# Optimization experiments

Measured on AMD Instinct MI355X. Metric: run time of the kernel, lower is better.

Reference implementation:

```python
import jax, jax.numpy as jnp
import numpy as np

N_NODES = 50000
N_GRAPHS = 512
EPS = 1e-5


def _ln(x, g, b):
    mu = jnp.mean(x, axis=-1, keepdims=True)
    var = jnp.var(x, axis=-1, keepdims=True)
    return (x - mu) * jax.lax.rsqrt(var + EPS) * g + b


def _sage(x, src, dst, wl, wr, bl):
    # mean-aggregate neighbor features: messages x[src] -> dst
    s = jax.ops.segment_sum(x[src], dst, num_segments=N_NODES)
    cnt = jax.ops.segment_sum(jnp.ones((src.shape[0],), x.dtype), dst, num_segments=N_NODES)
    agg = s / jnp.maximum(cnt, 1.0)[:, None]
    # PyG SAGEConv: lin_l(agg) + lin_r(x), bias only on lin_l
    return agg @ wl + bl + x @ wr


def setup_inputs() -> dict:
    key = jax.random.key(0)
    ks = jax.random.split(key, 16)
    C, H, NC, E = 128, 128, 2, 800000
    inp = {
        'x': jax.random.normal(ks[0], (N_NODES, C), jnp.float32),
        'edge_index': jax.random.randint(ks[1], (2, E), 0, N_NODES, jnp.int32),
        'batch': jnp.sort(jax.random.randint(ks[2], (N_NODES,), 0, N_GRAPHS, jnp.int32)),
    }
    def w(k, shape):
        return jax.random.normal(k, shape, jnp.float32) * 0.05
    inp.update({
        'w1l': w(ks[3], (C, H)), 'w1r': w(ks[4], (C, H)), 'b1': jnp.zeros((H,), jnp.float32),
        'g1': jnp.ones((H,), jnp.float32), 'be1': jnp.zeros((H,), jnp.float32),
        'w2l': w(ks[5], (H, H)), 'w2r': w(ks[6], (H, H)), 'b2': jnp.zeros((H,), jnp.float32),
        'g2': jnp.ones((H,), jnp.float32), 'be2': jnp.zeros((H,), jnp.float32),
        'w3l': w(ks[7], (H, H)), 'w3r': w(ks[8], (H, H)), 'b3': jnp.zeros((H,), jnp.float32),
        'g3': jnp.ones((H,), jnp.float32), 'be3': jnp.zeros((H,), jnp.float32),
        'wc': w(ks[9], (H, NC)), 'bc': jnp.zeros((NC,), jnp.float32),
    })
    return inp


def reference(x, edge_index, batch, w1l, w1r, b1, g1, be1, w2l, w2r, b2, g2, be2,
              w3l, w3r, b3, g3, be3, wc, bc):
    src, dst = edge_index[0], edge_index[1]
    # eval mode: dropout is identity
    h1 = _ln(jax.nn.relu(_sage(x, src, dst, w1l, w1r, b1)), g1, be1)
    h2 = _ln(jax.nn.relu(_sage(h1, src, dst, w2l, w2r, b2)) + h1, g2, be2)
    h3 = _ln(h2 + jax.nn.relu(_sage(h2, src, dst, w3l, w3r, b3)), g3, be3)
    # global mean pool over graphs
    s = jax.ops.segment_sum(h3, batch, num_segments=N_GRAPHS)
    cnt = jax.ops.segment_sum(jnp.ones((h3.shape[0],), h3.dtype), batch, num_segments=N_GRAPHS)
    avg = s / jnp.maximum(cnt, 1.0)[:, None]
    out = avg @ wc + bc
    return (out, h3, avg)
```

## Files before the change

### kernel.cpp

```cpp
#include <hip/hip_runtime.h>

#define NND 50000
#define NE  800000
#define CF  128
#define NGR 512
#define DCAP 64

typedef __bf16 bf16;
typedef __bf16 bf16x2 __attribute__((ext_vector_type(2)));
typedef __bf16 bf16x4 __attribute__((ext_vector_type(4)));
typedef __bf16 bf16x8 __attribute__((ext_vector_type(8)));
typedef float  f32x4  __attribute__((ext_vector_type(4)));

__device__ __forceinline__ int swz(int n, int k) {
  return n * 256 + (((k >> 3) ^ (n & 31)) << 3) + (k & 7);
}

__global__ __launch_bounds__(256) void conv_k(const float* __restrict__ x,
                                              bf16* __restrict__ xb,
                                              const float* __restrict__ w1l, const float* __restrict__ w1r,
                                              const float* __restrict__ w2l, const float* __restrict__ w2r,
                                              const float* __restrict__ w3l, const float* __restrict__ w3r,
                                              bf16* __restrict__ wb,
                                              const int* __restrict__ batch,
                                              int* __restrict__ gs,
                                              int* __restrict__ cnt) {
  int t = blockIdx.x * 256 + threadIdx.x;
  if (t < (NND * CF / 4)) {
    f32x4 v = ((const f32x4*)x)[t];
    bf16x4 o;
    o[0] = (bf16)v[0]; o[1] = (bf16)v[1]; o[2] = (bf16)v[2]; o[3] = (bf16)v[3];
    ((bf16x4*)xb)[t] = o;
  }
  if (t < 49152) {
    int m = t >> 13, w = t & 8191;
    const float* src = (m == 0) ? w1l : (m == 1) ? w1r : (m == 2) ? w2l
                     : (m == 3) ? w2r : (m == 4) ? w3l : w3r;
    float2 v = *(const float2*)(src + w * 2);
    bf16x2 o;
    o[0] = (bf16)v.x; o[1] = (bf16)v.y;
    ((bf16x2*)wb)[t] = o;
  }
  if (t < NND) {
    cnt[t] = 0;
    int b = batch[t];
    if (t == 0) {
      for (int g = 0; g <= b; g++) gs[g] = 0;
    } else {
      int pb = batch[t - 1];
      for (int g = pb + 1; g <= b; g++) gs[g] = t;
    }
    if (t == NND - 1) {
      for (int g = b + 1; g <= NGR; g++) gs[g] = NND;
    }
  }
}

__global__ __launch_bounds__(256) void fill_k(const int* __restrict__ src,
                                              const int* __restrict__ dst,
                                              int* __restrict__ cnt,
                                              unsigned short* __restrict__ csr) {
  int r  = blockIdx.x & 7;
  int lo = r * 6250, hi = lo + 6250;
  int base = (blockIdx.x >> 3) * 2048 + threadIdx.x * 8;
#pragma unroll
  for (int h = 0; h < 2; h++) {
    int e = base + h * 4;
    if (e < NE) {
      int4 d4 = *(const int4*)(dst + e);
      int dd[4] = {d4.x, d4.y, d4.z, d4.w};
#pragma unroll
      for (int u = 0; u < 4; u++) {
        int d = dd[u];
        if (d >= lo && d < hi) {
          int p = atomicAdd(&cnt[d], 1);
          if (p < DCAP) csr[d * DCAP + p] = (unsigned short)src[e + u];
        }
      }
    }
  }
}

__global__ __launch_bounds__(256) void agg_k(const bf16* __restrict__ xin,
                                             const int* __restrict__ cnt,
                                             const unsigned short* __restrict__ csr,
                                             bf16* __restrict__ aggout) {
  int wid  = (blockIdx.x * 256 + threadIdx.x) >> 6;
  int lane = threadIdx.x & 63;
  if (wid >= NND) return;
  int sub = lane >> 4;
  int c8  = (lane & 15) * 8;
  int deg = min(cnt[wid], DCAP);
  int ebase = wid * DCAP;
  float a[8] = {};
  {
    int s[8]; float m[8]; bf16x8 v[8];
#pragma unroll
    for (int u = 0; u < 4; u++) {
      int i = u * 4 + sub;
      s[u] = csr[ebase + ((i < deg) ? i : 0)];
      m[u] = (i < deg) ? 1.f : 0.f;
    }
#pragma unroll
    for (int u = 0; u < 4; u++) v[u] = *(const bf16x8*)(xin + s[u] * 128 + c8);
    if (deg > 16) {
#pragma unroll
      for (int u = 4; u < 8; u++) {
        int i = u * 4 + sub;
        s[u] = csr[ebase + ((i < deg) ? i : 0)];
        m[u] = (i < deg) ? 1.f : 0.f;
      }
#pragma unroll
      for (int u = 4; u < 8; u++) v[u] = *(const bf16x8*)(xin + s[u] * 128 + c8);
    }
#pragma unroll
    for (int u = 0; u < 4; u++)
#pragma unroll
      for (int j = 0; j < 8; j++) a[j] += m[u] * (float)v[u][j];
    if (deg > 16) {
#pragma unroll
      for (int u = 4; u < 8; u++)
#pragma unroll
        for (int j = 0; j < 8; j++) a[j] += m[u] * (float)v[u][j];
    }
  }
  for (int e = 32; e < deg; e += 16) {
    int s[4]; float m[4]; bf16x8 v[4];
#pragma unroll
    for (int u = 0; u < 4; u++) {
      int i = e + u * 4 + sub;
      s[u] = csr[ebase + ((i < deg) ? i : 0)];
      m[u] = (i < deg) ? 1.f : 0.f;
    }
#pragma unroll
    for (int u = 0; u < 4; u++) v[u] = *(const bf16x8*)(xin + s[u] * 128 + c8);
#pragma unroll
    for (int u = 0; u < 4; u++)
#pragma unroll
      for (int j = 0; j < 8; j++) a[j] += m[u] * (float)v[u][j];
  }
#pragma unroll
  for (int j = 0; j < 8; j++) {
    a[j] += __shfl_xor(a[j], 16);
    a[j] += __shfl_xor(a[j], 32);
  }
  if (sub == 0) {
    float inv = 1.0f / fmaxf((float)deg, 1.0f);
    bf16x8 o;
#pragma unroll
    for (int j = 0; j < 8; j++) o[j] = (bf16)(a[j] * inv);
    *(bf16x8*)(aggout + wid * 128 + c8) = o;
  }
}

template <typename TO>
__global__ __launch_bounds__(256, 2) void gemm_k(
    const bf16* __restrict__ aggp, const bf16* __restrict__ prev,
    const bf16* __restrict__ wl, const bf16* __restrict__ wr,
    const float* __restrict__ bias, const float* __restrict__ gamma,
    const float* __restrict__ beta, TO* __restrict__ outp, int addres) {
  __shared__ bf16 bt[128 * 256];
  int tid = threadIdx.x;
  for (int e = tid; e < 128 * 64; e += 256) {
    int k  = e >> 6;
    int n2 = (e & 63) << 1;
    {
      bf16x2 v = *(const bf16x2*)(wl + k * 128 + n2);
      bt[swz(n2, k)]     = v[0];
      bt[swz(n2 + 1, k)] = v[1];
    }
    {
      bf16x2 v = *(const bf16x2*)(wr + k * 128 + n2);
      bt[swz(n2, k + 128)]     = v[0];
      bt[swz(n2 + 1, k + 128)] = v[1];
    }
  }
  __syncthreads();

  int wave = tid >> 6, lane = tid & 63;
  int q = lane >> 4, r = lane & 15;
  int wrow = blockIdx.x * 128 + wave * 32;

  int arow[2];
#pragma unroll
  for (int rt = 0; rt < 2; rt++) {
    int ar = wrow + rt * 16 + r;
    arow[rt] = (ar < NND) ? ar : (NND - 1);
  }

  f32x4 acc[2][8] = {};

#pragma unroll
  for (int kk = 0; kk < 8; kk++) {
    int kof = kk * 32 + q * 8;
    bf16x8 af[2];
#pragma unroll
    for (int rt = 0; rt < 2; rt++) {
      const bf16* ap = (kk < 4) ? (aggp + arow[rt] * 128 + kof)
                                : (prev + arow[rt] * 128 + (kof - 128));
      af[rt] = *(const bf16x8*)ap;
    }
#pragma unroll
    for (int t = 0; t < 8; t++) {
      int n = t * 16 + r;
      bf16x8 bfrag = *(const bf16x8*)&bt[n * 256 + (((kof >> 3) ^ (n & 31)) << 3)];
#pragma unroll
      for (int rt = 0; rt < 2; rt++)
        acc[rt][t] = __builtin_amdgcn_mfma_f32_16x16x32_bf16(af[rt], bfrag, acc[rt][t], 0, 0, 0);
    }
  }

  float biasf[8], gf[8], bef[8];
#pragma unroll
  for (int t = 0; t < 8; t++) {
    int c = t * 16 + r;
    biasf[t] = bias[c];
    gf[t]    = gamma[c];
    bef[t]   = beta[c];
  }

#pragma unroll
  for (int rt = 0; rt < 2; rt++) {
#pragma unroll
    for (int reg = 0; reg < 4; reg++) {
      int row = wrow + rt * 16 + q * 4 + reg;
      int rr  = (row < NND) ? row : (NND - 1);
      const bf16* prow = prev + rr * 128;
      float vals[8];
      float s = 0.f, s2 = 0.f;
#pragma unroll
      for (int t = 0; t < 8; t++) {
        float v = acc[rt][t][reg] + biasf[t];
        v = fmaxf(v, 0.f);
        if (addres) v += (float)prow[t * 16 + r];
        vals[t] = v;
        s += v;
        s2 += v * v;
      }
#pragma unroll
      for (int m = 1; m < 16; m <<= 1) {
        s  += __shfl_xor(s, m);
        s2 += __shfl_xor(s2, m);
      }
      float mean = s * (1.f / 128.f);
      float var  = fmaxf(s2 * (1.f / 128.f) - mean * mean, 0.f);
      float rstd = rsqrtf(var + 1e-5f);
      if (row < NND) {
        TO* orow = outp + row * 128;
#pragma unroll
        for (int t = 0; t < 8; t++)
          orow[t * 16 + r] = (TO)((vals[t] - mean) * rstd * gf[t] + bef[t]);
      }
    }
  }
}

__global__ __launch_bounds__(256) void poolhead_k(
    const float* __restrict__ h3, const int* __restrict__ gs,
    const float* __restrict__ wc, const float* __restrict__ bc,
    float* __restrict__ outv, float* __restrict__ avgv) {
  int g = blockIdx.x;
  int s = gs[g], epos = gs[g + 1];
  int tid = threadIdx.x;
  int wave = tid >> 6, lane = tid & 63;
  float a0 = 0.f, a1 = 0.f;
  for (int row = s + wave; row < epos; row += 4) {
    float2 v = *(const float2*)(h3 + row * 128 + 2 * lane);
    a0 += v.x; a1 += v.y;
  }
  __shared__ float red[4][128];
  red[wave][2 * lane]     = a0;
  red[wave][2 * lane + 1] = a1;
  __syncthreads();
  __shared__ float sp[4];
  if (tid < 128) {
    float t4  = red[0][tid] + red[1][tid] + red[2][tid] + red[3][tid];
    float inv = 1.f / fmaxf((float)(epos - s), 1.f);
    float avg = t4 * inv;
    avgv[g * 128 + tid] = avg;
    float p0 = avg * wc[tid * 2 + 0];
    float p1 = avg * wc[tid * 2 + 1];
#pragma unroll
    for (int m = 1; m < 64; m <<= 1) {
      p0 += __shfl_xor(p0, m);
      p1 += __shfl_xor(p1, m);
    }
    if ((tid & 63) == 0) {
      sp[(tid >> 6) * 2]     = p0;
      sp[(tid >> 6) * 2 + 1] = p1;
    }
  }
  __syncthreads();
  if (tid == 0) {
    outv[g * 2 + 0] = sp[0] + sp[2] + bc[0];
    outv[g * 2 + 1] = sp[1] + sp[3] + bc[1];
  }
}

extern "C" void kernel_launch(void* const* d_in, const int* in_sizes, int n_in,
                              void* d_out, int out_size, void* d_ws, size_t ws_size,
                              hipStream_t stream) {
  const float* x   = (const float*)d_in[0];
  const int* ei    = (const int*)d_in[1];
  const int* batch = (const int*)d_in[2];
  const float* w1l = (const float*)d_in[3],  *w1r = (const float*)d_in[4];
  const float* b1  = (const float*)d_in[5],  *g1  = (const float*)d_in[6],  *be1 = (const float*)d_in[7];
  const float* w2l = (const float*)d_in[8],  *w2r = (const float*)d_in[9];
  const float* b2  = (const float*)d_in[10], *g2  = (const float*)d_in[11], *be2 = (const float*)d_in[12];
  const float* w3l = (const float*)d_in[13], *w3r = (const float*)d_in[14];
  const float* b3  = (const float*)d_in[15], *g3  = (const float*)d_in[16], *be3 = (const float*)d_in[17];
  const float* wc  = (const float*)d_in[18], *bc  = (const float*)d_in[19];
  const int* srcv = ei;
  const int* dstv = ei + NE;

  char* base = (char*)d_ws;
  int*            cnt  = (int*)(base + 0);
  int*            gs   = (int*)(base + 200064);
  bf16*           wb   = (bf16*)(base + 202752);
  unsigned short* csr  = (unsigned short*)(base + 399360);
  bf16*           agg  = (bf16*)(base + 6799360);
  bf16*           h1   = (bf16*)(base + 19599360);
  bf16*           h2xb = (bf16*)(base + 32399360);

  bf16* wb1l = wb,          *wb1r = wb + 16384;
  bf16* wb2l = wb + 32768,  *wb2r = wb + 49152;
  bf16* wb3l = wb + 65536,  *wb3r = wb + 81920;

  float* outv = (float*)d_out;
  float* h3   = outv + 1024;
  float* avgv = outv + 1024 + NND * CF;

  conv_k<<<6250, 256, 0, stream>>>(x, h2xb, w1l, w1r, w2l, w2r, w3l, w3r, wb, batch, gs, cnt);
  fill_k<<<3128, 256, 0, stream>>>(srcv, dstv, cnt, csr);

  agg_k<<<12500, 256, 0, stream>>>(h2xb, cnt, csr, agg);
  gemm_k<bf16><<<391, 256, 0, stream>>>(agg, h2xb, wb1l, wb1r, b1, g1, be1, h1, 0);
  agg_k<<<12500, 256, 0, stream>>>(h1, cnt, csr, agg);
  gemm_k<bf16><<<391, 256, 0, stream>>>(agg, h1, wb2l, wb2r, b2, g2, be2, h2xb, 1);
  agg_k<<<12500, 256, 0, stream>>>(h2xb, cnt, csr, agg);
  gemm_k<float><<<391, 256, 0, stream>>>(agg, h2xb, wb3l, wb3r, b3, g3, be3, h3, 1);
  poolhead_k<<<NGR, 256, 0, stream>>>(h3, gs, wc, bc, outv, avgv);
}
```

Measured before the change: 312.8 us.

## Fuse graph mean-pool into final GEMM epilogue and merge conversion with CSR fill

The last GEMM kernel now accumulates pooled per-graph sums in shared memory with atomics and flushes them to a global buffer, so pooling no longer needs to re-read h3. A small finish kernel then divides by node counts and applies the classifier head. The conversion and CSR-fill kernels are merged into one launch, with a separate zeroing kernel for the counters and pool buffer, and src is now read with vector loads. This trades an extra pass over h3 and a launch for shared and global float atomics, which add contention and make the summation order nondeterministic.

```diff
diff --git a/kernel.cpp b/kernel.cpp
--- a/kernel.cpp
+++ b/kernel.cpp
@@ -16,65 +16,71 @@
   return n * 256 + (((k >> 3) ^ (n & 31)) << 3) + (k & 7);
 }
 
-__global__ __launch_bounds__(256) void conv_k(const float* __restrict__ x,
-                                              bf16* __restrict__ xb,
-                                              const float* __restrict__ w1l, const float* __restrict__ w1r,
-                                              const float* __restrict__ w2l, const float* __restrict__ w2r,
-                                              const float* __restrict__ w3l, const float* __restrict__ w3r,
-                                              bf16* __restrict__ wb,
-                                              const int* __restrict__ batch,
-                                              int* __restrict__ gs,
-                                              int* __restrict__ cnt) {
-  int t = blockIdx.x * 256 + threadIdx.x;
-  if (t < (NND * CF / 4)) {
-    f32x4 v = ((const f32x4*)x)[t];
-    bf16x4 o;
-    o[0] = (bf16)v[0]; o[1] = (bf16)v[1]; o[2] = (bf16)v[2]; o[3] = (bf16)v[3];
-    ((bf16x4*)xb)[t] = o;
-  }
-  if (t < 49152) {
-    int m = t >> 13, w = t & 8191;
-    const float* src = (m == 0) ? w1l : (m == 1) ? w1r : (m == 2) ? w2l
-                     : (m == 3) ? w2r : (m == 4) ? w3l : w3r;
-    float2 v = *(const float2*)(src + w * 2);
-    bf16x2 o;
-    o[0] = (bf16)v.x; o[1] = (bf16)v.y;
-    ((bf16x2*)wb)[t] = o;
-  }
-  if (t < NND) {
-    cnt[t] = 0;
-    int b = batch[t];
-    if (t == 0) {
-      for (int g = 0; g <= b; g++) gs[g] = 0;
-    } else {
-      int pb = batch[t - 1];
-      for (int g = pb + 1; g <= b; g++) gs[g] = t;
-    }
-    if (t == NND - 1) {
-      for (int g = b + 1; g <= NGR; g++) gs[g] = NND;
-    }
-  }
-}
-
-__global__ __launch_bounds__(256) void fill_k(const int* __restrict__ src,
-                                              const int* __restrict__ dst,
-                                              int* __restrict__ cnt,
-                                              unsigned short* __restrict__ csr) {
-  int r  = blockIdx.x & 7;
-  int lo = r * 6250, hi = lo + 6250;
-  int base = (blockIdx.x >> 3) * 2048 + threadIdx.x * 8;
-#pragma unroll
-  for (int h = 0; h < 2; h++) {
-    int e = base + h * 4;
-    if (e < NE) {
-      int4 d4 = *(const int4*)(dst + e);
-      int dd[4] = {d4.x, d4.y, d4.z, d4.w};
-#pragma unroll
-      for (int u = 0; u < 4; u++) {
-        int d = dd[u];
-        if (d >= lo && d < hi) {
-          int p = atomicAdd(&cnt[d], 1);
-          if (p < DCAP) csr[d * DCAP + p] = (unsigned short)src[e + u];
+__global__ __launch_bounds__(256) void zero_k(int4* __restrict__ p) {
+  p[blockIdx.x * 256 + threadIdx.x] = int4{0, 0, 0, 0};
+}
+
+__global__ __launch_bounds__(256) void convfill_k(const float* __restrict__ x,
+                                                  bf16* __restrict__ xb,
+                                                  const float* __restrict__ w1l, const float* __restrict__ w1r,
+                                                  const float* __restrict__ w2l, const float* __restrict__ w2r,
+                                                  const float* __restrict__ w3l, const float* __restrict__ w3r,
+                                                  bf16* __restrict__ wb,
+                                                  const int* __restrict__ batch,
+                                                  int* __restrict__ gs,
+                                                  const int* __restrict__ src,
+                                                  const int* __restrict__ dst,
+                                                  int* __restrict__ cnt,
+                                                  unsigned short* __restrict__ csr) {
+  if (blockIdx.x < 6250) {
+    int t = blockIdx.x * 256 + threadIdx.x;
+    {
+      f32x4 v = ((const f32x4*)x)[t];
+      bf16x4 o;
+      o[0] = (bf16)v[0]; o[1] = (bf16)v[1]; o[2] = (bf16)v[2]; o[3] = (bf16)v[3];
+      ((bf16x4*)xb)[t] = o;
+    }
+    if (t < 49152) {
+      int m = t >> 13, w = t & 8191;
+      const float* sp = (m == 0) ? w1l : (m == 1) ? w1r : (m == 2) ? w2l
+                      : (m == 3) ? w2r : (m == 4) ? w3l : w3r;
+      float2 v = *(const float2*)(sp + w * 2);
+      bf16x2 o;
+      o[0] = (bf16)v.x; o[1] = (bf16)v.y;
+      ((bf16x2*)wb)[t] = o;
+    }
+    if (t < NND) {
+      int b = batch[t];
+      if (t == 0) {
+        for (int g = 0; g <= b; g++) gs[g] = 0;
+      } else {
+        int pb = batch[t - 1];
+        for (int g = pb + 1; g <= b; g++) gs[g] = t;
+      }
+      if (t == NND - 1) {
+        for (int g = b + 1; g <= NGR; g++) gs[g] = NND;
+      }
+    }
+  } else {
+    int bb = blockIdx.x - 6250;
+    int r  = bb & 7;
+    int lo = r * 6250, hi = lo + 6250;
+    int ebase = (bb >> 3) * 2048;
+#pragma unroll
+    for (int h = 0; h < 2; h++) {
+      int e = ebase + h * 1024 + threadIdx.x * 4;
+      if (e < NE) {
+        int4 d4 = *(const int4*)(dst + e);
+        int4 s4 = *(const int4*)(src + e);
+        int dd[4] = {d4.x, d4.y, d4.z, d4.w};
+        int ss[4] = {s4.x, s4.y, s4.z, s4.w};
+#pragma unroll
+        for (int u = 0; u < 4; u++) {
+          int d = dd[u];
+          if (d >= lo && d < hi) {
+            int p = atomicAdd(&cnt[d], 1);
+            if (p < DCAP) csr[d * DCAP + p] = (unsigned short)ss[u];
+          }
         }
       }
     }
@@ -158,7 +164,8 @@
     const bf16* __restrict__ aggp, const bf16* __restrict__ prev,
     const bf16* __restrict__ wl, const bf16* __restrict__ wr,
     const float* __restrict__ bias, const float* __restrict__ gamma,
-    const float* __restrict__ beta, TO* __restrict__ outp, int addres) {
+    const float* __restrict__ beta, TO* __restrict__ outp, int addres,
+    const int* __restrict__ batchp, float* __restrict__ avgsum, int dopool) {
   __shared__ bf16 bt[128 * 256];
   int tid = threadIdx.x;
   for (int e = tid; e < 128 * 64; e += 256) {
@@ -210,6 +217,18 @@
     }
   }
 
+  float* poolbuf = (float*)bt;
+  int gmin = 0, gspan = 0;
+  if (dopool) {
+    __syncthreads();
+    int row0 = blockIdx.x * 128;
+    gmin  = batchp[row0];
+    int gmax = batchp[min(row0 + 127, NND - 1)];
+    gspan = gmax - gmin + 1;
+    for (int i = tid; i < gspan * 128; i += 256) poolbuf[i] = 0.f;
+    __syncthreads();
+  }
+
   float biasf[8], gf[8], bef[8];
 #pragma unroll
   for (int t = 0; t < 8; t++) {
@@ -247,48 +266,45 @@
       float rstd = rsqrtf(var + 1e-5f);
       if (row < NND) {
         TO* orow = outp + row * 128;
-#pragma unroll
-        for (int t = 0; t < 8; t++)
-          orow[t * 16 + r] = (TO)((vals[t] - mean) * rstd * gf[t] + bef[t]);
-      }
-    }
-  }
-}
-
-__global__ __launch_bounds__(256) void poolhead_k(
-    const float* __restrict__ h3, const int* __restrict__ gs,
+        int gb = dopool ? batchp[row] : 0;
+#pragma unroll
+        for (int t = 0; t < 8; t++) {
+          float o = (vals[t] - mean) * rstd * gf[t] + bef[t];
+          orow[t * 16 + r] = (TO)o;
+          if (dopool) atomicAdd(&poolbuf[(gb - gmin) * 128 + t * 16 + r], o);
+        }
+      }
+    }
+  }
+
+  if (dopool) {
+    __syncthreads();
+    for (int i = tid; i < gspan * 128; i += 256)
+      atomicAdd(&avgsum[gmin * 128 + i], poolbuf[i]);
+  }
+}
+
+__global__ __launch_bounds__(128) void poolfin_k(
+    const float* __restrict__ avgsum, const int* __restrict__ gs,
     const float* __restrict__ wc, const float* __restrict__ bc,
     float* __restrict__ outv, float* __restrict__ avgv) {
   int g = blockIdx.x;
-  int s = gs[g], epos = gs[g + 1];
   int tid = threadIdx.x;
-  int wave = tid >> 6, lane = tid & 63;
-  float a0 = 0.f, a1 = 0.f;
-  for (int row = s + wave; row < epos; row += 4) {
-    float2 v = *(const float2*)(h3 + row * 128 + 2 * lane);
-    a0 += v.x; a1 += v.y;
-  }
-  __shared__ float red[4][128];
-  red[wave][2 * lane]     = a0;
-  red[wave][2 * lane + 1] = a1;
-  __syncthreads();
+  float s = avgsum[g * 128 + tid];
+  int c = gs[g + 1] - gs[g];
+  float avg = s / fmaxf((float)c, 1.f);
+  avgv[g * 128 + tid] = avg;
+  float p0 = avg * wc[tid * 2 + 0];
+  float p1 = avg * wc[tid * 2 + 1];
+#pragma unroll
+  for (int m = 1; m < 64; m <<= 1) {
+    p0 += __shfl_xor(p0, m);
+    p1 += __shfl_xor(p1, m);
+  }
   __shared__ float sp[4];
-  if (tid < 128) {
-    float t4  = red[0][tid] + red[1][tid] + red[2][tid] + red[3][tid];
-    float inv = 1.f / fmaxf((float)(epos - s), 1.f);
-    float avg = t4 * inv;
-    avgv[g * 128 + tid] = avg;
-    float p0 = avg * wc[tid * 2 + 0];
-    float p1 = avg * wc[tid * 2 + 1];
-#pragma unroll
-    for (int m = 1; m < 64; m <<= 1) {
-      p0 += __shfl_xor(p0, m);
-      p1 += __shfl_xor(p1, m);
-    }
-    if ((tid & 63) == 0) {
-      sp[(tid >> 6) * 2]     = p0;
-      sp[(tid >> 6) * 2 + 1] = p1;
-    }
+  if ((tid & 63) == 0) {
+    sp[(tid >> 6) * 2]     = p0;
+    sp[(tid >> 6) * 2 + 1] = p1;
   }
   __syncthreads();
   if (tid == 0) {
@@ -314,13 +330,14 @@
   const int* dstv = ei + NE;
 
   char* base = (char*)d_ws;
-  int*            cnt  = (int*)(base + 0);
-  int*            gs   = (int*)(base + 200064);
-  bf16*           wb   = (bf16*)(base + 202752);
-  unsigned short* csr  = (unsigned short*)(base + 399360);
-  bf16*           agg  = (bf16*)(base + 6799360);
-  bf16*           h1   = (bf16*)(base + 19599360);
-  bf16*           h2xb = (bf16*)(base + 32399360);
+  int*            cnt    = (int*)(base + 0);
+  float*          avgsum = (float*)(base + 200704);
+  int*            gs     = (int*)(base + 462848);
+  bf16*           wb     = (bf16*)(base + 465408);
+  unsigned short* csr    = (unsigned short*)(base + 662016);
+  bf16*           agg    = (bf16*)(base + 7062016);
+  bf16*           h1     = (bf16*)(base + 19862016);
+  bf16*           h2xb   = (bf16*)(base + 32662016);
 
   bf16* wb1l = wb,          *wb1r = wb + 16384;
   bf16* wb2l = wb + 32768,  *wb2r = wb + 49152;
@@ -330,14 +347,18 @@
   float* h3   = outv + 1024;
   float* avgv = outv + 1024 + NND * CF;
 
-  conv_k<<<6250, 256, 0, stream>>>(x, h2xb, w1l, w1r, w2l, w2r, w3l, w3r, wb, batch, gs, cnt);
-  fill_k<<<3128, 256, 0, stream>>>(srcv, dstv, cnt, csr);
+  zero_k<<<113, 256, 0, stream>>>((int4*)base);
+  convfill_k<<<9378, 256, 0, stream>>>(x, h2xb, w1l, w1r, w2l, w2r, w3l, w3r, wb,
+                                       batch, gs, srcv, dstv, cnt, csr);
 
   agg_k<<<12500, 256, 0, stream>>>(h2xb, cnt, csr, agg);
-  gemm_k<bf16><<<391, 256, 0, stream>>>(agg, h2xb, wb1l, wb1r, b1, g1, be1, h1, 0);
+  gemm_k<bf16><<<391, 256, 0, stream>>>(agg, h2xb, wb1l, wb1r, b1, g1, be1, h1, 0,
+                                        nullptr, nullptr, 0);
   agg_k<<<12500, 256, 0, stream>>>(h1, cnt, csr, agg);
-  gemm_k<bf16><<<391, 256, 0, stream>>>(agg, h1, wb2l, wb2r, b2, g2, be2, h2xb, 1);
+  gemm_k<bf16><<<391, 256, 0, stream>>>(agg, h1, wb2l, wb2r, b2, g2, be2, h2xb, 1,
+                                        nullptr, nullptr, 0);
   agg_k<<<12500, 256, 0, stream>>>(h2xb, cnt, csr, agg);
-  gemm_k<float><<<391, 256, 0, stream>>>(agg, h2xb, wb3l, wb3r, b3, g3, be3, h3, 1);
-  poolhead_k<<<NGR, 256, 0, stream>>>(h3, gs, wc, bc, outv, avgv);
-}
+  gemm_k<float><<<391, 256, 0, stream>>>(agg, h2xb, wb3l, wb3r, b3, g3, be3, h3, 1,
+                                         batch, avgsum, 1);
+  poolfin_k<<<NGR, 128, 0, stream>>>(avgsum, gs, wc, bc, outv, avgv);
+}
```

Result: slower. 339.7 us (+8.6%).

## Pre-swizzle weights once, halve GEMM LDS tile, merge conversion and CSR fill

Applied to the files above, without the earlier changes.

Weights are now written once in the swizzled [n][k] layout during conversion, so each GEMM block only does vectorized copies into LDS. The tile drops to 64 rows with a 32KB LDS buffer, loaded in two halves (lin_l, then lin_r), which allows more resident blocks and twice as many blocks. The conversion and edge-fill kernels are merged into one launch, with a separate zeroing kernel for counts, and the fill now reads src with vectorized loads. The cost is extra syncs between the GEMM halves. The merge also relies on cnt being zeroed by the earlier launch, since the fill blocks in the same grid can no longer depend on it.

```diff
diff --git a/kernel.cpp b/kernel.cpp
--- a/kernel.cpp
+++ b/kernel.cpp
@@ -12,69 +12,73 @@
 typedef __bf16 bf16x8 __attribute__((ext_vector_type(8)));
 typedef float  f32x4  __attribute__((ext_vector_type(4)));
 
-__device__ __forceinline__ int swz(int n, int k) {
-  return n * 256 + (((k >> 3) ^ (n & 31)) << 3) + (k & 7);
-}
-
-__global__ __launch_bounds__(256) void conv_k(const float* __restrict__ x,
-                                              bf16* __restrict__ xb,
-                                              const float* __restrict__ w1l, const float* __restrict__ w1r,
-                                              const float* __restrict__ w2l, const float* __restrict__ w2r,
-                                              const float* __restrict__ w3l, const float* __restrict__ w3r,
-                                              bf16* __restrict__ wb,
-                                              const int* __restrict__ batch,
-                                              int* __restrict__ gs,
-                                              int* __restrict__ cnt) {
-  int t = blockIdx.x * 256 + threadIdx.x;
-  if (t < (NND * CF / 4)) {
-    f32x4 v = ((const f32x4*)x)[t];
-    bf16x4 o;
-    o[0] = (bf16)v[0]; o[1] = (bf16)v[1]; o[2] = (bf16)v[2]; o[3] = (bf16)v[3];
-    ((bf16x4*)xb)[t] = o;
-  }
-  if (t < 49152) {
-    int m = t >> 13, w = t & 8191;
-    const float* src = (m == 0) ? w1l : (m == 1) ? w1r : (m == 2) ? w2l
-                     : (m == 3) ? w2r : (m == 4) ? w3l : w3r;
-    float2 v = *(const float2*)(src + w * 2);
-    bf16x2 o;
-    o[0] = (bf16)v.x; o[1] = (bf16)v.y;
-    ((bf16x2*)wb)[t] = o;
-  }
-  if (t < NND) {
-    cnt[t] = 0;
-    int b = batch[t];
-    if (t == 0) {
-      for (int g = 0; g <= b; g++) gs[g] = 0;
-    } else {
-      int pb = batch[t - 1];
-      for (int g = pb + 1; g <= b; g++) gs[g] = t;
-    }
-    if (t == NND - 1) {
-      for (int g = b + 1; g <= NGR; g++) gs[g] = NND;
-    }
-  }
-}
-
-__global__ __launch_bounds__(256) void fill_k(const int* __restrict__ src,
-                                              const int* __restrict__ dst,
-                                              int* __restrict__ cnt,
-                                              unsigned short* __restrict__ csr) {
-  int r  = blockIdx.x & 7;
-  int lo = r * 6250, hi = lo + 6250;
-  int base = (blockIdx.x >> 3) * 2048 + threadIdx.x * 8;
-#pragma unroll
-  for (int h = 0; h < 2; h++) {
-    int e = base + h * 4;
-    if (e < NE) {
-      int4 d4 = *(const int4*)(dst + e);
-      int dd[4] = {d4.x, d4.y, d4.z, d4.w};
-#pragma unroll
-      for (int u = 0; u < 4; u++) {
-        int d = dd[u];
-        if (d >= lo && d < hi) {
-          int p = atomicAdd(&cnt[d], 1);
-          if (p < DCAP) csr[d * DCAP + p] = (unsigned short)src[e + u];
+__global__ __launch_bounds__(256) void zero_k(int4* __restrict__ p) {
+  p[blockIdx.x * 256 + threadIdx.x] = int4{0, 0, 0, 0};
+}
+
+__global__ __launch_bounds__(256) void convfill_k(const float* __restrict__ x,
+                                                  bf16* __restrict__ xb,
+                                                  const float* __restrict__ w1l, const float* __restrict__ w1r,
+                                                  const float* __restrict__ w2l, const float* __restrict__ w2r,
+                                                  const float* __restrict__ w3l, const float* __restrict__ w3r,
+                                                  bf16* __restrict__ wb,
+                                                  const int* __restrict__ batch,
+                                                  int* __restrict__ gs,
+                                                  const int* __restrict__ src,
+                                                  const int* __restrict__ dst,
+                                                  int* __restrict__ cnt,
+                                                  unsigned short* __restrict__ csr) {
+  if (blockIdx.x < 6250) {
+    int t = blockIdx.x * 256 + threadIdx.x;
+    {
+      f32x4 v = ((const f32x4*)x)[t];
+      bf16x4 o;
+      o[0] = (bf16)v[0]; o[1] = (bf16)v[1]; o[2] = (bf16)v[2]; o[3] = (bf16)v[3];
+      ((bf16x4*)xb)[t] = o;
+    }
+    if (t < 49152) {
+      int m = t >> 13, w2 = t & 8191;
+      const float* sp = (m == 0) ? w1l : (m == 1) ? w1r : (m == 2) ? w2l
+                      : (m == 3) ? w2r : (m == 4) ? w3l : w3r;
+      int e0 = w2 * 2;
+      int k = e0 >> 7, n = e0 & 127;
+      float2 v = *(const float2*)(sp + e0);
+      bf16* wm = wb + m * 16384;
+      wm[n * 128       + ((((k >> 3) ^ (n       & 15)) << 3)) + (k & 7)] = (bf16)v.x;
+      wm[(n + 1) * 128 + ((((k >> 3) ^ ((n + 1) & 15)) << 3)) + (k & 7)] = (bf16)v.y;
+    }
+    if (t < NND) {
+      int b = batch[t];
+      if (t == 0) {
+        for (int g = 0; g <= b; g++) gs[g] = 0;
+      } else {
+        int pb = batch[t - 1];
+        for (int g = pb + 1; g <= b; g++) gs[g] = t;
+      }
+      if (t == NND - 1) {
+        for (int g = b + 1; g <= NGR; g++) gs[g] = NND;
+      }
+    }
+  } else {
+    int bb = blockIdx.x - 6250;
+    int r  = bb & 7;
+    int lo = r * 6250, hi = lo + 6250;
+    int ebase = (bb >> 3) * 2048;
+#pragma unroll
+    for (int h = 0; h < 2; h++) {
+      int e = ebase + h * 1024 + threadIdx.x * 4;
+      if (e < NE) {
+        int4 d4 = *(const int4*)(dst + e);
+        int4 s4 = *(const int4*)(src + e);
+        int dd[4] = {d4.x, d4.y, d4.z, d4.w};
+        int ss[4] = {s4.x, s4.y, s4.z, s4.w};
+#pragma unroll
+        for (int u = 0; u < 4; u++) {
+          int d = dd[u];
+          if (d >= lo && d < hi) {
+            int p = atomicAdd(&cnt[d], 1);
+            if (p < DCAP) csr[d * DCAP + p] = (unsigned short)ss[u];
+          }
         }
       }
     }
@@ -154,59 +158,61 @@
 }
 
 template <typename TO>
-__global__ __launch_bounds__(256, 2) void gemm_k(
+__global__ __launch_bounds__(256, 4) void gemm_k(
     const bf16* __restrict__ aggp, const bf16* __restrict__ prev,
-    const bf16* __restrict__ wl, const bf16* __restrict__ wr,
+    const bf16* __restrict__ wswz,
     const float* __restrict__ bias, const float* __restrict__ gamma,
     const float* __restrict__ beta, TO* __restrict__ outp, int addres) {
-  __shared__ bf16 bt[128 * 256];
+  __shared__ bf16 bt[16384];
   int tid = threadIdx.x;
-  for (int e = tid; e < 128 * 64; e += 256) {
-    int k  = e >> 6;
-    int n2 = (e & 63) << 1;
-    {
-      bf16x2 v = *(const bf16x2*)(wl + k * 128 + n2);
-      bt[swz(n2, k)]     = v[0];
-      bt[swz(n2 + 1, k)] = v[1];
-    }
-    {
-      bf16x2 v = *(const bf16x2*)(wr + k * 128 + n2);
-      bt[swz(n2, k + 128)]     = v[0];
-      bt[swz(n2 + 1, k + 128)] = v[1];
-    }
-  }
-  __syncthreads();
-
-  int wave = tid >> 6, lane = tid & 63;
+  int lane = tid & 63;
+  int wave = tid >> 6;
   int q = lane >> 4, r = lane & 15;
-  int wrow = blockIdx.x * 128 + wave * 32;
-
-  int arow[2];
-#pragma unroll
-  for (int rt = 0; rt < 2; rt++) {
-    int ar = wrow + rt * 16 + r;
-    arow[rt] = (ar < NND) ? ar : (NND - 1);
-  }
-
-  f32x4 acc[2][8] = {};
-
-#pragma unroll
-  for (int kk = 0; kk < 8; kk++) {
-    int kof = kk * 32 + q * 8;
-    bf16x8 af[2];
-#pragma unroll
-    for (int rt = 0; rt < 2; rt++) {
-      const bf16* ap = (kk < 4) ? (aggp + arow[rt] * 128 + kof)
-                                : (prev + arow[rt] * 128 + (kof - 128));
-      af[rt] = *(const bf16x8*)ap;
-    }
+  int wrow = blockIdx.x * 64 + wave * 16;
+  int arow = min(wrow + r, NND - 1);
+
+  {
+    const bf16x8* g = (const bf16x8*)wswz;
+#pragma unroll
+    for (int i = 0; i < 8; i++)
+      ((bf16x8*)bt)[tid + i * 256] = g[tid + i * 256];
+  }
+  bf16x8 af0[4], af1[4];
+  {
+    const bf16* a0 = aggp + arow * 128 + q * 8;
+    const bf16* a1 = prev + arow * 128 + q * 8;
+#pragma unroll
+    for (int kk = 0; kk < 4; kk++) af0[kk] = *(const bf16x8*)(a0 + kk * 32);
+#pragma unroll
+    for (int kk = 0; kk < 4; kk++) af1[kk] = *(const bf16x8*)(a1 + kk * 32);
+  }
+  __syncthreads();
+
+  f32x4 acc[8] = {};
+#pragma unroll
+  for (int kk = 0; kk < 4; kk++) {
 #pragma unroll
     for (int t = 0; t < 8; t++) {
       int n = t * 16 + r;
-      bf16x8 bfrag = *(const bf16x8*)&bt[n * 256 + (((kof >> 3) ^ (n & 31)) << 3)];
-#pragma unroll
-      for (int rt = 0; rt < 2; rt++)
-        acc[rt][t] = __builtin_amdgcn_mfma_f32_16x16x32_bf16(af[rt], bfrag, acc[rt][t], 0, 0, 0);
+      bf16x8 bfrag = *(const bf16x8*)&bt[n * 128 + (((kk * 4 + q) ^ (n & 15)) << 3)];
+      acc[t] = __builtin_amdgcn_mfma_f32_16x16x32_bf16(af0[kk], bfrag, acc[t], 0, 0, 0);
+    }
+  }
+  __syncthreads();
+  {
+    const bf16x8* g = (const bf16x8*)(wswz + 16384);
+#pragma unroll
+    for (int i = 0; i < 8; i++)
+      ((bf16x8*)bt)[tid + i * 256] = g[tid + i * 256];
+  }
+  __syncthreads();
+#pragma unroll
+  for (int kk = 0; kk < 4; kk++) {
+#pragma unroll
+    for (int t = 0; t < 8; t++) {
+      int n = t * 16 + r;
+      bf16x8 bfrag = *(const bf16x8*)&bt[n * 128 + (((kk * 4 + q) ^ (n & 15)) << 3)];
+      acc[t] = __builtin_amdgcn_mfma_f32_16x16x32_bf16(af1[kk], bfrag, acc[t], 0, 0, 0);
     }
   }
 
@@ -220,37 +226,34 @@
   }
 
 #pragma unroll
-  for (int rt = 0; rt < 2; rt++) {
-#pragma unroll
-    for (int reg = 0; reg < 4; reg++) {
-      int row = wrow + rt * 16 + q * 4 + reg;
-      int rr  = (row < NND) ? row : (NND - 1);
-      const bf16* prow = prev + rr * 128;
-      float vals[8];
-      float s = 0.f, s2 = 0.f;
-#pragma unroll
-      for (int t = 0; t < 8; t++) {
-        float v = acc[rt][t][reg] + biasf[t];
-        v = fmaxf(v, 0.f);
-        if (addres) v += (float)prow[t * 16 + r];
-        vals[t] = v;
-        s += v;
-        s2 += v * v;
-      }
-#pragma unroll
-      for (int m = 1; m < 16; m <<= 1) {
-        s  += __shfl_xor(s, m);
-        s2 += __shfl_xor(s2, m);
-      }
-      float mean = s * (1.f / 128.f);
-      float var  = fmaxf(s2 * (1.f / 128.f) - mean * mean, 0.f);
-      float rstd = rsqrtf(var + 1e-5f);
-      if (row < NND) {
-        TO* orow = outp + row * 128;
-#pragma unroll
-        for (int t = 0; t < 8; t++)
-          orow[t * 16 + r] = (TO)((vals[t] - mean) * rstd * gf[t] + bef[t]);
-      }
+  for (int reg = 0; reg < 4; reg++) {
+    int row = wrow + q * 4 + reg;
+    int rr  = (row < NND) ? row : (NND - 1);
+    const bf16* prow = prev + rr * 128;
+    float vals[8];
+    float s = 0.f, s2 = 0.f;
+#pragma unroll
+    for (int t = 0; t < 8; t++) {
+      float v = acc[t][reg] + biasf[t];
+      v = fmaxf(v, 0.f);
+      if (addres) v += (float)prow[t * 16 + r];
+      vals[t] = v;
+      s += v;
+      s2 += v * v;
+    }
+#pragma unroll
+    for (int m = 1; m < 16; m <<= 1) {
+      s  += __shfl_xor(s, m);
+      s2 += __shfl_xor(s2, m);
+    }
+    float mean = s * (1.f / 128.f);
+    float var  = fmaxf(s2 * (1.f / 128.f) - mean * mean, 0.f);
+    float rstd = rsqrtf(var + 1e-5f);
+    if (row < NND) {
+      TO* orow = outp + row * 128;
+#pragma unroll
+      for (int t = 0; t < 8; t++)
+        orow[t * 16 + r] = (TO)((vals[t] - mean) * rstd * gf[t] + bef[t]);
     }
   }
 }
@@ -315,29 +318,26 @@
 
   char* base = (char*)d_ws;
   int*            cnt  = (int*)(base + 0);
-  int*            gs   = (int*)(base + 200064);
-  bf16*           wb   = (bf16*)(base + 202752);
-  unsigned short* csr  = (unsigned short*)(base + 399360);
-  bf16*           agg  = (bf16*)(base + 6799360);
-  bf16*           h1   = (bf16*)(base + 19599360);
-  bf16*           h2xb = (bf16*)(base + 32399360);
-
-  bf16* wb1l = wb,          *wb1r = wb + 16384;
-  bf16* wb2l = wb + 32768,  *wb2r = wb + 49152;
-  bf16* wb3l = wb + 65536,  *wb3r = wb + 81920;
+  int*            gs   = (int*)(base + 200704);
+  bf16*           wb   = (bf16*)(base + 204800);
+  unsigned short* csr  = (unsigned short*)(base + 401408);
+  bf16*           agg  = (bf16*)(base + 6801408);
+  bf16*           h1   = (bf16*)(base + 19601408);
+  bf16*           h2xb = (bf16*)(base + 32401408);
 
   float* outv = (float*)d_out;
   float* h3   = outv + 1024;
   float* avgv = outv + 1024 + NND * CF;
 
-  conv_k<<<6250, 256, 0, stream>>>(x, h2xb, w1l, w1r, w2l, w2r, w3l, w3r, wb, batch, gs, cnt);
-  fill_k<<<3128, 256, 0, stream>>>(srcv, dstv, cnt, csr);
+  zero_k<<<49, 256, 0, stream>>>((int4*)base);
+  convfill_k<<<9378, 256, 0, stream>>>(x, h2xb, w1l, w1r, w2l, w2r, w3l, w3r, wb,
+                                       batch, gs, srcv, dstv, cnt, csr);
 
   agg_k<<<12500, 256, 0, stream>>>(h2xb, cnt, csr, agg);
-  gemm_k<bf16><<<391, 256, 0, stream>>>(agg, h2xb, wb1l, wb1r, b1, g1, be1, h1, 0);
+  gemm_k<bf16><<<782, 256, 0, stream>>>(agg, h2xb, wb,           b1, g1, be1, h1, 0);
   agg_k<<<12500, 256, 0, stream>>>(h1, cnt, csr, agg);
-  gemm_k<bf16><<<391, 256, 0, stream>>>(agg, h1, wb2l, wb2r, b2, g2, be2, h2xb, 1);
+  gemm_k<bf16><<<782, 256, 0, stream>>>(agg, h1, wb + 2 * 16384, b2, g2, be2, h2xb, 1);
   agg_k<<<12500, 256, 0, stream>>>(h2xb, cnt, csr, agg);
-  gemm_k<float><<<391, 256, 0, stream>>>(agg, h2xb, wb3l, wb3r, b3, g3, be3, h3, 1);
+  gemm_k<float><<<782, 256, 0, stream>>>(agg, h2xb, wb + 4 * 16384, b3, g3, be3, h3, 1);
   poolhead_k<<<NGR, 256, 0, stream>>>(h3, gs, wc, bc, outv, avgv);
 }
```

Result: faster. 290.9 us (-7.0%).
